# Performance work log

Hardware: AMD Instinct MI355X
Metric: run time of the kernel (lower is better)

Reference implementation:

```python
import jax, jax.numpy as jnp
import numpy as np

B, T = 8, 1024
D = 256          # n_embd
NH = 4           # n_head
MULT = 4         # mlp_internal_dim_multiplier
GRID = 32        # grid_size, T == GRID*GRID
NLAYER = 3
N = D * MULT // NH   # sparse head dim = 256
EPS = 1e-5


def _freqs_2d(h, w, dim, theta=10000.0):
    # matches get_freqs_2d_fixed: returns (h*w, dim//2) complex64
    dim_half = dim // 2
    freqs = 1.0 / theta ** (np.arange(0, dim_half, 2, dtype=np.float32) / dim_half)
    fx = np.outer(np.arange(w, dtype=np.float32), freqs)
    fy = np.outer(np.arange(h, dtype=np.float32), freqs)
    cx = np.exp(1j * fx).astype(np.complex64)          # (w, dim_half/2)
    cy = np.exp(1j * fy).astype(np.complex64)          # (h, dim_half/2)
    gx = np.broadcast_to(cx[None, :, :], (h, w, cx.shape[-1]))
    gy = np.broadcast_to(cy[:, None, :], (h, w, cy.shape[-1]))
    return np.concatenate([gx, gy], axis=-1).reshape(h * w, -1)

FREQS = jnp.asarray(_freqs_2d(GRID, GRID, N))  # (T, N//2) complex64


def _rope(x):
    # x: (B, nh, T, N) real -> complex pairs, rotate, back to real
    xc = x.reshape(*x.shape[:-1], -1, 2)
    xc = jax.lax.complex(xc[..., 0], xc[..., 1])       # (B, nh, T, N/2)
    xr = xc * FREQS[None, None, :, :]
    out = jnp.stack([jnp.real(xr), jnp.imag(xr)], axis=-1)
    return out.reshape(x.shape).astype(x.dtype)


def _ln(x):
    # LayerNorm over last dim, no affine (biased variance, like torch)
    m = jnp.mean(x, axis=-1, keepdims=True)
    v = jnp.var(x, axis=-1, keepdims=True)
    return (x - m) / jnp.sqrt(v + EPS)


def setup_inputs() -> dict:
    key = jax.random.key(0)
    ks = jax.random.split(key, 6)
    std = 0.02
    return {
        "inputs": jax.random.normal(ks[0], (B, T), dtype=jnp.float32),
        "in_w": jax.random.normal(ks[1], (D, 1), dtype=jnp.float32) * std,
        "in_b": jnp.zeros((D,), dtype=jnp.float32),
        "encoder": jax.random.normal(ks[2], (NH, D, N), dtype=jnp.float32) * std,
        "encoder_v": jax.random.normal(ks[3], (NH, D, N), dtype=jnp.float32) * std,
        "decoder": jax.random.normal(ks[4], (NH * N, D), dtype=jnp.float32) * std,
        "out_w": jax.random.normal(ks[5], (1, D), dtype=jnp.float32) * std,
        "out_b": jnp.zeros((1,), dtype=jnp.float32),
    }


def reference(inputs, in_w, in_b, encoder, encoder_v, decoder, out_w, out_b):
    # input projection: (B,T,1) @ (1,D) + b -> (B,T,D)
    x = inputs[..., None] * in_w[None, None, :, 0].swapaxes(-1, -1)  # placeholder
    x = inputs[..., None] @ in_w.T + in_b                            # (B,T,D)
    x = _ln(x)
    scale = 1.0 / jnp.sqrt(jnp.asarray(N, dtype=x.dtype))
    for _ in range(NLAYER):
        # encoder: (B,T,D) x (nh,D,N) -> (B,nh,T,N)
        x_sparse = jax.nn.relu(jnp.einsum('btd,hdn->bhtn', x, encoder))
        QR = _rope(x_sparse)
        KR = _rope(x_sparse)
        scores = jnp.einsum('bhtn,bhsn->bhts', QR, KR) * scale       # (B,nh,T,T)
        attn = jax.nn.softmax(scores, axis=-1)
        yKV = jnp.einsum('bhts,bsd->bhtd', attn, x)                  # V = x, broadcast over heads
        yKV = _ln(yKV)
        y_sparse = jax.nn.relu(jnp.einsum('bhtd,hdn->bhtn', yKV, encoder_v))
        xy_sparse = x_sparse * y_sparse                              # (B,nh,T,N)
        # (B,nh,T,N) -> (B,T,nh*N) @ (nh*N,D) -> (B,T,D)
        yMLP = xy_sparse.transpose(0, 2, 1, 3).reshape(B, T, NH * N) @ decoder
        x = _ln(x + _ln(yMLP))
    logits = x @ out_w.T + out_b                                     # (B,T,1)
    return logits
```

## Files before the change

### kernel.cpp

```cpp
#include <hip/hip_runtime.h>
#include <hip/hip_bf16.h>
#include <math.h>

#define B_ 8
#define T_ 1024
#define D_ 256
#define NH_ 4
#define N_ 256
#define EPS_ 1e-5f

typedef __attribute__((ext_vector_type(8))) short short8_t;
typedef __attribute__((ext_vector_type(4))) float floatx4;

__device__ inline unsigned short f2bf(float f) {
    unsigned u = __builtin_bit_cast(unsigned, f);
    u += 0x7FFFu + ((u >> 16) & 1u);
    return (unsigned short)(u >> 16);
}
__device__ inline float bf2f(unsigned short h) {
    return __builtin_bit_cast(float, (unsigned)h << 16);
}

__device__ inline void gload_lds16(const unsigned short* g, unsigned short* l) {
    __builtin_amdgcn_global_load_lds(
        (const __attribute__((address_space(1))) unsigned int*)g,
        (__attribute__((address_space(3))) unsigned int*)l, 16, 0, 0);
}

__device__ inline float2 block_stats_256(float v, float* red) {
    float s1 = v, s2 = v * v;
    #pragma unroll
    for (int o = 32; o > 0; o >>= 1) { s1 += __shfl_down(s1, o); s2 += __shfl_down(s2, o); }
    int wave = threadIdx.x >> 6, lane = threadIdx.x & 63;
    __syncthreads();
    if (lane == 0) { red[wave] = s1; red[4 + wave] = s2; }
    __syncthreads();
    float S1 = red[0] + red[1] + red[2] + red[3];
    float S2 = red[4] + red[5] + red[6] + red[7];
    float mean = S1 * (1.f / 256.f);
    float var  = S2 * (1.f / 256.f) - mean * mean;
    return make_float2(mean, var);
}

__global__ __launch_bounds__(256) void k_wT(
    const float* __restrict__ in, unsigned short* __restrict__ outh,
    unsigned short* __restrict__ outl, int R, int C)
{
    __shared__ float tile[64][65];
    int c0 = blockIdx.x * 64, r0 = blockIdx.y * 64, h = blockIdx.z;
    in += (size_t)h * R * C;
    for (int i = threadIdx.x; i < 4096; i += 256) {
        int r = i >> 6, c = i & 63;
        tile[r][c] = in[(size_t)(r0 + r) * C + c0 + c];
    }
    __syncthreads();
    for (int i = threadIdx.x; i < 4096; i += 256) {
        int c = i >> 6, r = i & 63;
        float v = tile[r][c];
        unsigned short hb = f2bf(v);
        size_t o = (size_t)(h * C + c0 + c) * R + r0 + r;
        outh[o] = hb;
        outl[o] = f2bf(v - bf2f(hb));
    }
}

__global__ __launch_bounds__(256) void k_input_ln(
    const float* __restrict__ inputs, const float* __restrict__ in_w,
    const float* __restrict__ in_b, float* __restrict__ x,
    unsigned short* __restrict__ xh, unsigned short* __restrict__ xl)
{
    __shared__ float red[8];
    int row = blockIdx.x;
    int d = threadIdx.x;
    float v = inputs[row] * in_w[d] + in_b[d];
    float2 mv = block_stats_256(v, red);
    float o = (v - mv.x) * rsqrtf(mv.y + EPS_);
    size_t idx = (size_t)row * D_ + d;
    x[idx] = o;
    unsigned short hb = f2bf(o);
    xh[idx] = hb;
    xl[idx] = f2bf(o - bf2f(hb));
}

template<int MODE>
__global__ __launch_bounds__(256, 2) void k_gemm_mfma(
    const unsigned short* __restrict__ Ah, const unsigned short* __restrict__ Al,
    const unsigned short* __restrict__ Wh, const unsigned short* __restrict__ Wl,
    const unsigned short* __restrict__ xsh, const unsigned short* __restrict__ xsl,
    unsigned short* __restrict__ outh, unsigned short* __restrict__ outl,
    float* __restrict__ outf,
    unsigned short* __restrict__ qrh, unsigned short* __restrict__ qrl)
{
    constexpr int K = (MODE == 2) ? 1024 : 256;
    __shared__ unsigned short As_h[8 * 512], As_l[8 * 512];
    __shared__ unsigned short Ws_h[8 * 512], Ws_l[8 * 512];
    int tid = threadIdx.x;
    int w = tid >> 6, lane = tid & 63, quad = lane >> 4, l16 = lane & 15;
    int wm = w >> 1, wn = w & 1;
    int m0 = blockIdx.y * 128, n0x = blockIdx.x * 128;
    size_t a_row0, w_row0, out_row0;
    int col0;
    int koff = 0, kend = K;
    if (MODE == 1) {
        int bh = blockIdx.z;
        a_row0 = (size_t)bh * 1024 + m0;
        w_row0 = (size_t)((bh & 3) * 256 + n0x);
        out_row0 = (size_t)(bh >> 2) * 1024 + m0;
        col0 = (bh & 3) * 256 + n0x;
    } else {
        a_row0 = m0; w_row0 = n0x; out_row0 = m0; col0 = n0x;
        if (MODE == 2) { koff = blockIdx.z * 256; kend = koff + 256; }
    }
    floatx4 acc[4][4];
    #pragma unroll
    for (int mt = 0; mt < 4; mt++)
        #pragma unroll
        for (int nt = 0; nt < 4; nt++)
            acc[mt][nt] = (floatx4){0.f, 0.f, 0.f, 0.f};

    const unsigned short* ssrc = (w == 0) ? Ah : (w == 1) ? Al : (w == 2) ? Wh : Wl;
    unsigned short* sdst = (w == 0) ? As_h : (w == 1) ? As_l : (w == 2) ? Ws_h : Ws_l;
    size_t srow0 = (w < 2) ? a_row0 : w_row0;

    for (int k0 = koff; k0 < kend; k0 += 32) {
        #pragma unroll
        for (int rt = 0; rt < 8; rt++) {
            size_t g = (srow0 + rt * 16 + l16) * (size_t)K + k0 + quad * 8;
            gload_lds16(ssrc + g, sdst + rt * 512);
        }
        __syncthreads();
        short8_t afh[4], afl[4], bfh[4], bfl[4];
        #pragma unroll
        for (int mt = 0; mt < 4; mt++) {
            afh[mt] = *(const short8_t*)&As_h[(wm * 4 + mt) * 512 + lane * 8];
            afl[mt] = *(const short8_t*)&As_l[(wm * 4 + mt) * 512 + lane * 8];
        }
        #pragma unroll
        for (int nt = 0; nt < 4; nt++) {
            bfh[nt] = *(const short8_t*)&Ws_h[(wn * 4 + nt) * 512 + lane * 8];
            bfl[nt] = *(const short8_t*)&Ws_l[(wn * 4 + nt) * 512 + lane * 8];
        }
        #pragma unroll
        for (int mt = 0; mt < 4; mt++)
            #pragma unroll
            for (int nt = 0; nt < 4; nt++) {
                acc[mt][nt] = __builtin_amdgcn_mfma_f32_16x16x32_bf16(afh[mt], bfh[nt], acc[mt][nt], 0, 0, 0);
                acc[mt][nt] = __builtin_amdgcn_mfma_f32_16x16x32_bf16(afh[mt], bfl[nt], acc[mt][nt], 0, 0, 0);
                acc[mt][nt] = __builtin_amdgcn_mfma_f32_16x16x32_bf16(afl[mt], bfh[nt], acc[mt][nt], 0, 0, 0);
            }
        __syncthreads();
    }

    #pragma unroll
    for (int mt = 0; mt < 4; mt++) {
        #pragma unroll
        for (int r = 0; r < 4; r++) {
            size_t grow = out_row0 + wm * 64 + mt * 16 + quad * 4 + r;
            #pragma unroll
            for (int nt = 0; nt < 4; nt++) {
                int gcol = col0 + wn * 64 + nt * 16 + l16;
                float v = acc[mt][nt][r];
                if (MODE == 0) {
                    v = fmaxf(v, 0.f);
                    size_t o = grow * 1024 + gcol;
                    unsigned short hb = f2bf(v);
                    outh[o] = hb;
                    outl[o] = f2bf(v - bf2f(hb));
                    float vp = __shfl_xor(v, 1);
                    int n = gcol & 255, h = gcol >> 8;
                    int t = (int)(grow & 1023), b = (int)(grow >> 10);
                    int p = n >> 1, j = p & 63;
                    int pos = (p < 64) ? (t & 31) : (t >> 5);
                    float f = __expf((float)j * -0.14391156f);
                    float ang = (float)pos * f;
                    float sn = __sinf(ang), cs = __cosf(ang);
                    float ro = (n & 1) ? (vp * sn + v * cs) : (v * cs - vp * sn);
                    size_t qo = (((size_t)b * NH_ + h) * T_ + t) * N_ + n;
                    unsigned short qb = f2bf(ro);
                    qrh[qo] = qb;
                    qrl[qo] = f2bf(ro - bf2f(qb));
                } else if (MODE == 1) {
                    float y = fmaxf(v, 0.f);
                    size_t o = grow * 1024 + gcol;
                    float xv = bf2f(xsh[o]) + bf2f(xsl[o]);
                    float p = xv * y;
                    unsigned short hb = f2bf(p);
                    outh[o] = hb;
                    outl[o] = f2bf(p - bf2f(hb));
                } else {
                    outf[(size_t)blockIdx.z * 2097152 + grow * 256 + gcol] = v;
                }
            }
        }
    }
}

__global__ __launch_bounds__(256) void k_xT(const float* __restrict__ x,
                                            unsigned short* __restrict__ Vfh,
                                            unsigned short* __restrict__ Vfl)
{
    __shared__ float tile[64][65];
    int t0 = blockIdx.x * 64, d0 = blockIdx.y * 64, b = blockIdx.z;
    const float* src = x + ((size_t)b * T_ + t0) * D_ + d0;
    for (int i = threadIdx.x; i < 1024; i += 256) {
        int r = i >> 4, c = i & 15;
        float4 v = *(const float4*)(src + (size_t)r * D_ + c * 4);
        tile[r][c * 4 + 0] = v.x;
        tile[r][c * 4 + 1] = v.y;
        tile[r][c * 4 + 2] = v.z;
        tile[r][c * 4 + 3] = v.w;
    }
    __syncthreads();
    for (int i = threadIdx.x; i < 1024; i += 256) {
        int d = i >> 4, c = i & 15;
        int tg = t0 + c * 4;
        int jj = tg >> 5, qd = (tg >> 3) & 3, i8 = tg & 7;
        int dg = d0 + d;
        int tn = dg >> 4, s16 = dg & 15;
        size_t o = (((size_t)b * 32 + jj) * 16 + tn) * 512 + (qd * 16 + s16) * 8 + i8;
        float v0 = tile[c * 4 + 0][d], v1 = tile[c * 4 + 1][d];
        float v2 = tile[c * 4 + 2][d], v3 = tile[c * 4 + 3][d];
        ushort4 oh, ol;
        oh.x = f2bf(v0); ol.x = f2bf(v0 - bf2f(oh.x));
        oh.y = f2bf(v1); ol.y = f2bf(v1 - bf2f(oh.y));
        oh.z = f2bf(v2); ol.z = f2bf(v2 - bf2f(oh.z));
        oh.w = f2bf(v3); ol.w = f2bf(v3 - bf2f(oh.w));
        *(ushort4*)(Vfh + o) = oh;
        *(ushort4*)(Vfl + o) = ol;
    }
}

#define PPW2 36

__global__ __launch_bounds__(512, 1) void k_attn_mfma(
    const unsigned short* __restrict__ qr_h, const unsigned short* __restrict__ qr_l,
    const unsigned short* __restrict__ Vf_h, const unsigned short* __restrict__ Vf_l,
    unsigned short* __restrict__ ykvh, unsigned short* __restrict__ ykvl)
{
    __shared__ unsigned short K_h[2][16 * 512];
    __shared__ unsigned short K_l[2][16 * 512];
    __shared__ unsigned short V_h[2][16 * 512];
    __shared__ unsigned short V_l[2][16 * 512];
    __shared__ unsigned short P_h[4][32 * PPW2];
    __shared__ unsigned short P_l[4][32 * PPW2];
    __shared__ float l_scr[8][32];
    __shared__ float s1_scr[8][32];
    __shared__ float s2_scr[8][32];

    int tid = threadIdx.x;
    int w = tid >> 6, lane = tid & 63, quad = lane >> 4, l16 = lane & 15;
    int rg = w >> 1, half = w & 1;
    int gid = blockIdx.x;
    int bh = gid & 31, tile = gid >> 5, b = bh >> 2;
    int t0q = tile * 128;
    const unsigned short* qhb = qr_h + (size_t)bh * T_ * N_;
    const unsigned short* qlb = qr_l + (size_t)bh * T_ * N_;
    const unsigned short* vhb = Vf_h + (size_t)b * 32 * 16 * 512;
    const unsigned short* vlb = Vf_l + (size_t)b * 32 * 16 * 512;

    short8_t qfh[2][8], qfl[2][8];
    #pragma unroll
    for (int mt = 0; mt < 2; mt++)
        #pragma unroll
        for (int kc = 0; kc < 8; kc++) {
            size_t o = (size_t)(t0q + rg * 32 + mt * 16 + l16) * N_ + kc * 32 + quad * 8;
            qfh[mt][kc] = *(const short8_t*)(qhb + o);
            qfl[mt][kc] = *(const short8_t*)(qlb + o);
        }

    floatx4 O[2][8];
    #pragma unroll
    for (int mt = 0; mt < 2; mt++)
        #pragma unroll
        for (int t = 0; t < 8; t++) O[mt][t] = (floatx4){0.f, 0.f, 0.f, 0.f};
    float lst[2][4] = {{0.f, 0.f, 0.f, 0.f}, {0.f, 0.f, 0.f, 0.f}};
    const float scale = 0.0625f;

    #pragma unroll
    for (int s = 0; s < 2; s++) {
        int slot = w * 2 + s;
        int ct = slot >> 3, kc = slot & 7;
        size_t go = (size_t)(ct * 16 + l16) * N_ + kc * 32 + quad * 8;
        gload_lds16(qhb + go, &K_h[0][slot * 512]);
        gload_lds16(qlb + go, &K_l[0][slot * 512]);
        size_t vo = ((size_t)slot << 9) + lane * 8;
        gload_lds16(vhb + vo, &V_h[0][slot * 512]);
        gload_lds16(vlb + vo, &V_l[0][slot * 512]);
    }

    for (int j = 0; j < 32; j++) {
        int buf = j & 1;
        __syncthreads();
        if (j < 31) {
            #pragma unroll
            for (int s = 0; s < 2; s++) {
                int slot = w * 2 + s;
                size_t vo = ((size_t)((j + 1) * 16 + slot) << 9) + lane * 8;
                gload_lds16(vhb + vo, &V_h[buf ^ 1][slot * 512]);
                gload_lds16(vlb + vo, &V_l[buf ^ 1][slot * 512]);
            }
        }

        floatx4 a_hh0 = (floatx4){0.f, 0.f, 0.f, 0.f};
        floatx4 a_hl0 = (floatx4){0.f, 0.f, 0.f, 0.f};
        floatx4 a_lh0 = (floatx4){0.f, 0.f, 0.f, 0.f};
        floatx4 a_hh1 = (floatx4){0.f, 0.f, 0.f, 0.f};
        floatx4 a_hl1 = (floatx4){0.f, 0.f, 0.f, 0.f};
        floatx4 a_lh1 = (floatx4){0.f, 0.f, 0.f, 0.f};
        __builtin_amdgcn_s_setprio(1);
        #pragma unroll
        for (int kc = 0; kc < 8; kc++) {
            short8_t bkh = *(const short8_t*)&K_h[buf][(half * 8 + kc) * 512 + lane * 8];
            short8_t bkl = *(const short8_t*)&K_l[buf][(half * 8 + kc) * 512 + lane * 8];
            a_hh0 = __builtin_amdgcn_mfma_f32_16x16x32_bf16(qfh[0][kc], bkh, a_hh0, 0, 0, 0);
            a_hh1 = __builtin_amdgcn_mfma_f32_16x16x32_bf16(qfh[1][kc], bkh, a_hh1, 0, 0, 0);
            a_hl0 = __builtin_amdgcn_mfma_f32_16x16x32_bf16(qfh[0][kc], bkl, a_hl0, 0, 0, 0);
            a_hl1 = __builtin_amdgcn_mfma_f32_16x16x32_bf16(qfh[1][kc], bkl, a_hl1, 0, 0, 0);
            a_lh0 = __builtin_amdgcn_mfma_f32_16x16x32_bf16(qfl[0][kc], bkh, a_lh0, 0, 0, 0);
            a_lh1 = __builtin_amdgcn_mfma_f32_16x16x32_bf16(qfl[1][kc], bkh, a_lh1, 0, 0, 0);
        }
        __builtin_amdgcn_s_setprio(0);
        floatx4 sc0 = (a_hh0 + a_hl0) + a_lh0;
        floatx4 sc1 = (a_hh1 + a_hl1) + a_lh1;

        #pragma unroll
        for (int r = 0; r < 4; r++) {
            float p0 = __expf(sc0[r] * scale - 8.f);
            float p1 = __expf(sc1[r] * scale - 8.f);
            lst[0][r] += p0;
            lst[1][r] += p1;
            int row0 = quad * 4 + r, row1 = 16 + quad * 4 + r;
            unsigned short p0h = f2bf(p0), p1h = f2bf(p1);
            P_h[rg][row0 * PPW2 + half * 16 + l16] = p0h;
            P_h[rg][row1 * PPW2 + half * 16 + l16] = p1h;
            P_l[rg][row0 * PPW2 + half * 16 + l16] = f2bf(p0 - bf2f(p0h));
            P_l[rg][row1 * PPW2 + half * 16 + l16] = f2bf(p1 - bf2f(p1h));
        }

        __syncthreads();
        if (j < 31) {
            #pragma unroll
            for (int s = 0; s < 2; s++) {
                int slot = w * 2 + s;
                int ct = slot >> 3, kc = slot & 7;
                size_t go = (size_t)((j + 1) * 32 + ct * 16 + l16) * N_ + kc * 32 + quad * 8;
                gload_lds16(qhb + go, &K_h[buf ^ 1][slot * 512]);
                gload_lds16(qlb + go, &K_l[buf ^ 1][slot * 512]);
            }
        }

        short8_t pah0 = *(const short8_t*)&P_h[rg][(l16) * PPW2 + quad * 8];
        short8_t pal0 = *(const short8_t*)&P_l[rg][(l16) * PPW2 + quad * 8];
        short8_t pah1 = *(const short8_t*)&P_h[rg][(16 + l16) * PPW2 + quad * 8];
        short8_t pal1 = *(const short8_t*)&P_l[rg][(16 + l16) * PPW2 + quad * 8];

        __builtin_amdgcn_s_setprio(1);
        #pragma unroll
        for (int t = 0; t < 8; t++) {
            int tn = half * 8 + t;
            short8_t vbh = *(const short8_t*)&V_h[buf][tn * 512 + lane * 8];
            short8_t vbl = *(const short8_t*)&V_l[buf][tn * 512 + lane * 8];
            O[0][t] = __builtin_amdgcn_mfma_f32_16x16x32_bf16(pah0, vbh, O[0][t], 0, 0, 0);
            O[1][t] = __builtin_amdgcn_mfma_f32_16x16x32_bf16(pah1, vbh, O[1][t], 0, 0, 0);
            O[0][t] = __builtin_amdgcn_mfma_f32_16x16x32_bf16(pah0, vbl, O[0][t], 0, 0, 0);
            O[1][t] = __builtin_amdgcn_mfma_f32_16x16x32_bf16(pah1, vbl, O[1][t], 0, 0, 0);
            O[0][t] = __builtin_amdgcn_mfma_f32_16x16x32_bf16(pal0, vbh, O[0][t], 0, 0, 0);
            O[1][t] = __builtin_amdgcn_mfma_f32_16x16x32_bf16(pal1, vbh, O[1][t], 0, 0, 0);
        }
        __builtin_amdgcn_s_setprio(0);
    }

    #pragma unroll
    for (int mt = 0; mt < 2; mt++)
        #pragma unroll
        for (int r = 0; r < 4; r++) {
            float ls = lst[mt][r];
            #pragma unroll
            for (int o = 1; o < 16; o <<= 1) ls += __shfl_xor(ls, o);
            float s1 = 0.f, s2 = 0.f;
            #pragma unroll
            for (int t = 0; t < 8; t++) { float v = O[mt][t][r]; s1 += v; s2 += v * v; }
            #pragma unroll
            for (int o = 1; o < 16; o <<= 1) { s1 += __shfl_xor(s1, o); s2 += __shfl_xor(s2, o); }
            int row = mt * 16 + quad * 4 + r;
            if (l16 == 0) { l_scr[w][row] = ls; s1_scr[w][row] = s1; s2_scr[w][row] = s2; }
        }
    __syncthreads();
    #pragma unroll
    for (int mt = 0; mt < 2; mt++)
        #pragma unroll
        for (int r = 0; r < 4; r++) {
            int row = mt * 16 + quad * 4 + r;
            float ls = l_scr[w][row] + l_scr[w ^ 1][row];
            float s1 = s1_scr[w][row] + s1_scr[w ^ 1][row];
            float s2 = s2_scr[w][row] + s2_scr[w ^ 1][row];
            float li = 1.f / ls;
            float mean = s1 * li * (1.f / 256.f);
            float e2   = s2 * li * li * (1.f / 256.f);
            float var  = e2 - mean * mean;
            float rs = rsqrtf(var + EPS_);
            float a = li * rs, bb = mean * rs;
            size_t obase = ((size_t)bh * T_ + t0q + rg * 32 + row) * D_;
            #pragma unroll
            for (int t = 0; t < 8; t++) {
                float v = O[mt][t][r] * a - bb;
                size_t o = obase + half * 128 + t * 16 + l16;
                unsigned short hb = f2bf(v);
                ykvh[o] = hb;
                ykvl[o] = f2bf(v - bf2f(hb));
            }
        }
}

__global__ __launch_bounds__(256) void k_resid_ln(float* __restrict__ x,
                                                  const float* __restrict__ ymlp,
                                                  unsigned short* __restrict__ xh,
                                                  unsigned short* __restrict__ xl)
{
    __shared__ float red[8];
    int row = blockIdx.x, d = threadIdx.x;
    size_t o = (size_t)row * D_ + d;
    float y = ymlp[o] + ymlp[o + 2097152] + ymlp[o + 2 * 2097152] + ymlp[o + 3 * 2097152];
    float2 mv1 = block_stats_256(y, red);
    float v = x[o] + (y - mv1.x) * rsqrtf(mv1.y + EPS_);
    float2 mv2 = block_stats_256(v, red);
    float out = (v - mv2.x) * rsqrtf(mv2.y + EPS_);
    x[o] = out;
    unsigned short hb = f2bf(out);
    xh[o] = hb;
    xl[o] = f2bf(out - bf2f(hb));
}

__global__ __launch_bounds__(256) void k_logits(
    const float* __restrict__ x, const float* __restrict__ out_w,
    const float* __restrict__ out_b, float* __restrict__ out)
{
    __shared__ float red[4];
    int row = blockIdx.x, d = threadIdx.x;
    float v = x[(size_t)row * D_ + d] * out_w[d];
    #pragma unroll
    for (int o = 32; o > 0; o >>= 1) v += __shfl_down(v, o);
    int wave = d >> 6, lane = d & 63;
    if (lane == 0) red[wave] = v;
    __syncthreads();
    if (d == 0) out[row] = red[0] + red[1] + red[2] + red[3] + out_b[0];
}

extern "C" void kernel_launch(void* const* d_in, const int* in_sizes, int n_in,
                              void* d_out, int out_size, void* d_ws, size_t ws_size,
                              hipStream_t stream)
{
    (void)in_sizes; (void)n_in; (void)out_size;
    if (ws_size < ((size_t)115 << 20)) return;

    const float* inputs    = (const float*)d_in[0];
    const float* in_w      = (const float*)d_in[1];
    const float* in_b      = (const float*)d_in[2];
    const float* encoder   = (const float*)d_in[3];
    const float* encoder_v = (const float*)d_in[4];
    const float* decoder   = (const float*)d_in[5];
    const float* out_w     = (const float*)d_in[6];
    const float* out_b     = (const float*)d_in[7];

    char* wsb = (char*)d_ws;
    float* x             = (float*)(wsb);
    unsigned short* x_h  = (unsigned short*)(wsb + ((size_t)8  << 20));
    unsigned short* x_l  = (unsigned short*)(wsb + ((size_t)12 << 20));
    unsigned short* Vf_h = x_h;
    unsigned short* Vf_l = x_l;
    unsigned short* xs_h = (unsigned short*)(wsb + ((size_t)16 << 20));
    unsigned short* xs_l = (unsigned short*)(wsb + ((size_t)32 << 20));
    float* ymlp          = (float*)(wsb + ((size_t)16 << 20));
    unsigned short* qr_h = (unsigned short*)(wsb + ((size_t)48 << 20));
    unsigned short* qr_l = (unsigned short*)(wsb + ((size_t)64 << 20));
    unsigned short* xy_h = qr_h;
    unsigned short* xy_l = qr_l;
    unsigned short* ykv_h = (unsigned short*)(wsb + ((size_t)80 << 20));
    unsigned short* ykv_l = (unsigned short*)(wsb + ((size_t)96 << 20));
    char* wbase = wsb + ((size_t)112 << 20);
    unsigned short* encT_h = (unsigned short*)(wbase);
    unsigned short* encT_l = (unsigned short*)(wbase + 0x80000);
    unsigned short* evT_h  = (unsigned short*)(wbase + 2 * 0x80000);
    unsigned short* evT_l  = (unsigned short*)(wbase + 3 * 0x80000);
    unsigned short* decT_h = (unsigned short*)(wbase + 4 * 0x80000);
    unsigned short* decT_l = (unsigned short*)(wbase + 5 * 0x80000);

    k_wT<<<dim3(4, 4, 4), 256, 0, stream>>>(encoder,   encT_h, encT_l, 256, 256);
    k_wT<<<dim3(4, 4, 4), 256, 0, stream>>>(encoder_v, evT_h,  evT_l,  256, 256);
    k_wT<<<dim3(4, 16, 1), 256, 0, stream>>>(decoder,  decT_h, decT_l, 1024, 256);

    k_input_ln<<<B_ * T_, 256, 0, stream>>>(inputs, in_w, in_b, x, x_h, x_l);
    for (int l = 0; l < 3; l++) {
        k_gemm_mfma<0><<<dim3(8, 64, 1), 256, 0, stream>>>(
            x_h, x_l, encT_h, encT_l, nullptr, nullptr, xs_h, xs_l, nullptr, qr_h, qr_l);
        k_xT<<<dim3(16, 4, 8), 256, 0, stream>>>(x, Vf_h, Vf_l);
        k_attn_mfma<<<256, 512, 0, stream>>>(qr_h, qr_l, Vf_h, Vf_l, ykv_h, ykv_l);
        k_gemm_mfma<1><<<dim3(2, 8, 32), 256, 0, stream>>>(
            ykv_h, ykv_l, evT_h, evT_l, xs_h, xs_l, xy_h, xy_l, nullptr, nullptr, nullptr);
        k_gemm_mfma<2><<<dim3(2, 64, 4), 256, 0, stream>>>(
            xy_h, xy_l, decT_h, decT_l, nullptr, nullptr, nullptr, nullptr, ymlp, nullptr, nullptr);
        k_resid_ln<<<B_ * T_, 256, 0, stream>>>(x, ymlp, x_h, x_l);
    }
    k_logits<<<B_ * T_, 256, 0, stream>>>(x, out_w, out_b, (float*)d_out);
}
```

Before: 732.4 us.

## Fuse encoder_v GEMM, gating product, and decoder GEMM into one kernel

Replaces the separate encoder_v GEMM (MODE 1) and decoder GEMM (MODE 2) with one fused kernel. Each 512-thread block computes a full 128x256 y_sparse tile, multiplies it by x_sparse, and writes the bf16 hi/lo product straight into LDS as the A operand of the decoder GEMM, so the xy_sparse tensor never round-trips through global memory. Both GEMM phases use double-buffered LDS staging so global loads overlap MFMA. The cost is a grid of only 256 blocks at one block per CU, larger LDS use, and per-head partial outputs that resid_ln still has to sum.

```diff
diff --git a/kernel.cpp b/kernel.cpp
--- a/kernel.cpp
+++ b/kernel.cpp
@@ -86,31 +86,18 @@
 __global__ __launch_bounds__(256, 2) void k_gemm_mfma(
     const unsigned short* __restrict__ Ah, const unsigned short* __restrict__ Al,
     const unsigned short* __restrict__ Wh, const unsigned short* __restrict__ Wl,
-    const unsigned short* __restrict__ xsh, const unsigned short* __restrict__ xsl,
     unsigned short* __restrict__ outh, unsigned short* __restrict__ outl,
-    float* __restrict__ outf,
     unsigned short* __restrict__ qrh, unsigned short* __restrict__ qrl)
 {
-    constexpr int K = (MODE == 2) ? 1024 : 256;
+    constexpr int K = 256;
     __shared__ unsigned short As_h[8 * 512], As_l[8 * 512];
     __shared__ unsigned short Ws_h[8 * 512], Ws_l[8 * 512];
     int tid = threadIdx.x;
     int w = tid >> 6, lane = tid & 63, quad = lane >> 4, l16 = lane & 15;
     int wm = w >> 1, wn = w & 1;
     int m0 = blockIdx.y * 128, n0x = blockIdx.x * 128;
-    size_t a_row0, w_row0, out_row0;
-    int col0;
-    int koff = 0, kend = K;
-    if (MODE == 1) {
-        int bh = blockIdx.z;
-        a_row0 = (size_t)bh * 1024 + m0;
-        w_row0 = (size_t)((bh & 3) * 256 + n0x);
-        out_row0 = (size_t)(bh >> 2) * 1024 + m0;
-        col0 = (bh & 3) * 256 + n0x;
-    } else {
-        a_row0 = m0; w_row0 = n0x; out_row0 = m0; col0 = n0x;
-        if (MODE == 2) { koff = blockIdx.z * 256; kend = koff + 256; }
-    }
+    size_t a_row0 = m0, w_row0 = n0x, out_row0 = m0;
+    int col0 = n0x;
     floatx4 acc[4][4];
     #pragma unroll
     for (int mt = 0; mt < 4; mt++)
@@ -122,7 +109,7 @@
     unsigned short* sdst = (w == 0) ? As_h : (w == 1) ? As_l : (w == 2) ? Ws_h : Ws_l;
     size_t srow0 = (w < 2) ? a_row0 : w_row0;
 
-    for (int k0 = koff; k0 < kend; k0 += 32) {
+    for (int k0 = 0; k0 < K; k0 += 32) {
         #pragma unroll
         for (int rt = 0; rt < 8; rt++) {
             size_t g = (srow0 + rt * 16 + l16) * (size_t)K + k0 + quad * 8;
@@ -160,39 +147,170 @@
             for (int nt = 0; nt < 4; nt++) {
                 int gcol = col0 + wn * 64 + nt * 16 + l16;
                 float v = acc[mt][nt][r];
-                if (MODE == 0) {
-                    v = fmaxf(v, 0.f);
-                    size_t o = grow * 1024 + gcol;
-                    unsigned short hb = f2bf(v);
-                    outh[o] = hb;
-                    outl[o] = f2bf(v - bf2f(hb));
-                    float vp = __shfl_xor(v, 1);
-                    int n = gcol & 255, h = gcol >> 8;
-                    int t = (int)(grow & 1023), b = (int)(grow >> 10);
-                    int p = n >> 1, j = p & 63;
-                    int pos = (p < 64) ? (t & 31) : (t >> 5);
-                    float f = __expf((float)j * -0.14391156f);
-                    float ang = (float)pos * f;
-                    float sn = __sinf(ang), cs = __cosf(ang);
-                    float ro = (n & 1) ? (vp * sn + v * cs) : (v * cs - vp * sn);
-                    size_t qo = (((size_t)b * NH_ + h) * T_ + t) * N_ + n;
-                    unsigned short qb = f2bf(ro);
-                    qrh[qo] = qb;
-                    qrl[qo] = f2bf(ro - bf2f(qb));
-                } else if (MODE == 1) {
-                    float y = fmaxf(v, 0.f);
+                v = fmaxf(v, 0.f);
+                size_t o = grow * 1024 + gcol;
+                unsigned short hb = f2bf(v);
+                outh[o] = hb;
+                outl[o] = f2bf(v - bf2f(hb));
+                float vp = __shfl_xor(v, 1);
+                int n = gcol & 255, h = gcol >> 8;
+                int t = (int)(grow & 1023), b = (int)(grow >> 10);
+                int p = n >> 1, j = p & 63;
+                int pos = (p < 64) ? (t & 31) : (t >> 5);
+                float f = __expf((float)j * -0.14391156f);
+                float ang = (float)pos * f;
+                float sn = __sinf(ang), cs = __cosf(ang);
+                float ro = (n & 1) ? (vp * sn + v * cs) : (v * cs - vp * sn);
+                size_t qo = (((size_t)b * NH_ + h) * T_ + t) * N_ + n;
+                unsigned short qb = f2bf(ro);
+                qrh[qo] = qb;
+                qrl[qo] = f2bf(ro - bf2f(qb));
+            }
+        }
+    }
+}
+
+__global__ __launch_bounds__(512, 1) void k_gemm_fused(
+    const unsigned short* __restrict__ Ah, const unsigned short* __restrict__ Al,
+    const unsigned short* __restrict__ Wh, const unsigned short* __restrict__ Wl,
+    const unsigned short* __restrict__ D2h, const unsigned short* __restrict__ D2l,
+    const unsigned short* __restrict__ xsh, const unsigned short* __restrict__ xsl,
+    float* __restrict__ outf)
+{
+    __shared__ unsigned short SM[2][24576];
+    int tid = threadIdx.x;
+    int w = tid >> 6, lane = tid & 63, quad = lane >> 4, l16 = lane & 15;
+    int wm = w >> 2, wn = w & 3;
+    int m0 = blockIdx.x * 128;
+    int bh = blockIdx.y, b = bh >> 2, h = bh & 3;
+    size_t a_row0 = (size_t)bh * 1024 + m0;
+    size_t w_row0 = (size_t)h * 256;
+    size_t xrow0  = (size_t)b * 1024 + m0;
+
+    floatx4 acc[4][4];
+    #pragma unroll
+    for (int mt = 0; mt < 4; mt++)
+        #pragma unroll
+        for (int nt = 0; nt < 4; nt++)
+            acc[mt][nt] = (floatx4){0.f, 0.f, 0.f, 0.f};
+
+    auto stage_main = [&](int k0, int bw) {
+        #pragma unroll
+        for (int t = 0; t < 6; t++) {
+            int idx = w * 6 + t;
+            const unsigned short* src; unsigned short* dst; size_t rowb; int rt;
+            if (idx < 8)       { rt = idx;      src = Ah; dst = &SM[bw][0];     rowb = a_row0; }
+            else if (idx < 16) { rt = idx - 8;  src = Al; dst = &SM[bw][4096];  rowb = a_row0; }
+            else if (idx < 32) { rt = idx - 16; src = Wh; dst = &SM[bw][8192];  rowb = w_row0; }
+            else               { rt = idx - 32; src = Wl; dst = &SM[bw][16384]; rowb = w_row0; }
+            gload_lds16(src + (rowb + rt * 16 + l16) * 256 + k0 + quad * 8, dst + rt * 512);
+        }
+    };
+
+    stage_main(0, 0);
+    for (int s = 0; s < 8; s++) {
+        int buf = s & 1;
+        __syncthreads();
+        if (s < 7) stage_main((s + 1) * 32, buf ^ 1);
+        short8_t afh[4], afl[4], bfh[4], bfl[4];
+        #pragma unroll
+        for (int mt = 0; mt < 4; mt++) {
+            afh[mt] = *(const short8_t*)&SM[buf][(wm * 4 + mt) * 512 + lane * 8];
+            afl[mt] = *(const short8_t*)&SM[buf][4096 + (wm * 4 + mt) * 512 + lane * 8];
+        }
+        #pragma unroll
+        for (int nt = 0; nt < 4; nt++) {
+            bfh[nt] = *(const short8_t*)&SM[buf][8192  + (wn * 4 + nt) * 512 + lane * 8];
+            bfl[nt] = *(const short8_t*)&SM[buf][16384 + (wn * 4 + nt) * 512 + lane * 8];
+        }
+        #pragma unroll
+        for (int mt = 0; mt < 4; mt++)
+            #pragma unroll
+            for (int nt = 0; nt < 4; nt++) {
+                acc[mt][nt] = __builtin_amdgcn_mfma_f32_16x16x32_bf16(afh[mt], bfh[nt], acc[mt][nt], 0, 0, 0);
+                acc[mt][nt] = __builtin_amdgcn_mfma_f32_16x16x32_bf16(afh[mt], bfl[nt], acc[mt][nt], 0, 0, 0);
+                acc[mt][nt] = __builtin_amdgcn_mfma_f32_16x16x32_bf16(afl[mt], bfh[nt], acc[mt][nt], 0, 0, 0);
+            }
+    }
+
+    auto write_xy = [&](int c, int bw) {
+        if (wn != (c >> 1)) return;
+        int cb = c & 1;
+        #pragma unroll
+        for (int mt = 0; mt < 4; mt++)
+            #pragma unroll
+            for (int nt = 0; nt < 4; nt++) {
+                if ((nt >> 1) != cb) continue;
+                #pragma unroll
+                for (int r = 0; r < 4; r++) {
+                    float v = fmaxf(acc[mt][nt][r], 0.f);
+                    size_t grow = xrow0 + wm * 64 + mt * 16 + quad * 4 + r;
+                    int gcol = h * 256 + wn * 64 + nt * 16 + l16;
                     size_t o = grow * 1024 + gcol;
                     float xv = bf2f(xsh[o]) + bf2f(xsl[o]);
-                    float p = xv * y;
-                    unsigned short hb = f2bf(p);
-                    outh[o] = hb;
-                    outl[o] = f2bf(p - bf2f(hb));
-                } else {
-                    outf[(size_t)blockIdx.z * 2097152 + grow * 256 + gcol] = v;
+                    float p = xv * v;
+                    unsigned short ph = f2bf(p);
+                    int kin = (nt & 1) * 16 + l16;
+                    int ad = (wm * 4 + mt) * 512 + (kin >> 3) * 128 + (quad * 4 + r) * 8 + (kin & 7);
+                    SM[bw][ad] = ph;
+                    SM[bw][4096 + ad] = f2bf(p - bf2f(ph));
                 }
             }
-        }
-    }
+    };
+    auto stage_w2 = [&](int c, int bw) {
+        #pragma unroll
+        for (int t = 0; t < 4; t++) {
+            int idx = w * 4 + t;
+            const unsigned short* src = (idx < 16) ? D2h : D2l;
+            unsigned short* dst = (idx < 16) ? &SM[bw][8192] : &SM[bw][16384];
+            int rt = idx & 15;
+            gload_lds16(src + (size_t)(rt * 16 + l16) * 1024 + h * 256 + c * 32 + quad * 8,
+                        dst + rt * 512);
+        }
+    };
+
+    floatx4 acc2[4][4];
+    #pragma unroll
+    for (int mt = 0; mt < 4; mt++)
+        #pragma unroll
+        for (int nt = 0; nt < 4; nt++)
+            acc2[mt][nt] = (floatx4){0.f, 0.f, 0.f, 0.f};
+
+    write_xy(0, 0);
+    stage_w2(0, 0);
+    #pragma unroll
+    for (int c = 0; c < 8; c++) {
+        int buf = c & 1;
+        __syncthreads();
+        if (c < 7) { write_xy(c + 1, buf ^ 1); stage_w2(c + 1, buf ^ 1); }
+        short8_t b2h[4], b2l[4];
+        #pragma unroll
+        for (int nt = 0; nt < 4; nt++) {
+            b2h[nt] = *(const short8_t*)&SM[buf][8192  + (wn * 4 + nt) * 512 + lane * 8];
+            b2l[nt] = *(const short8_t*)&SM[buf][16384 + (wn * 4 + nt) * 512 + lane * 8];
+        }
+        #pragma unroll
+        for (int mt = 0; mt < 4; mt++) {
+            short8_t a2h = *(const short8_t*)&SM[buf][(wm * 4 + mt) * 512 + lane * 8];
+            short8_t a2l = *(const short8_t*)&SM[buf][4096 + (wm * 4 + mt) * 512 + lane * 8];
+            #pragma unroll
+            for (int nt = 0; nt < 4; nt++) {
+                acc2[mt][nt] = __builtin_amdgcn_mfma_f32_16x16x32_bf16(a2h, b2h[nt], acc2[mt][nt], 0, 0, 0);
+                acc2[mt][nt] = __builtin_amdgcn_mfma_f32_16x16x32_bf16(a2h, b2l[nt], acc2[mt][nt], 0, 0, 0);
+                acc2[mt][nt] = __builtin_amdgcn_mfma_f32_16x16x32_bf16(a2l, b2h[nt], acc2[mt][nt], 0, 0, 0);
+            }
+        }
+    }
+
+    #pragma unroll
+    for (int mt = 0; mt < 4; mt++)
+        #pragma unroll
+        for (int r = 0; r < 4; r++) {
+            size_t grow = xrow0 + wm * 64 + mt * 16 + quad * 4 + r;
+            #pragma unroll
+            for (int nt = 0; nt < 4; nt++)
+                outf[(size_t)h * 2097152 + grow * 256 + wn * 64 + nt * 16 + l16] = acc2[mt][nt][r];
+        }
 }
 
 __global__ __launch_bounds__(256) void k_xT(const float* __restrict__ x,
@@ -470,11 +588,9 @@
     unsigned short* Vf_l = x_l;
     unsigned short* xs_h = (unsigned short*)(wsb + ((size_t)16 << 20));
     unsigned short* xs_l = (unsigned short*)(wsb + ((size_t)32 << 20));
-    float* ymlp          = (float*)(wsb + ((size_t)16 << 20));
     unsigned short* qr_h = (unsigned short*)(wsb + ((size_t)48 << 20));
     unsigned short* qr_l = (unsigned short*)(wsb + ((size_t)64 << 20));
-    unsigned short* xy_h = qr_h;
-    unsigned short* xy_l = qr_l;
+    float* ymlp          = (float*)(wsb + ((size_t)48 << 20));
     unsigned short* ykv_h = (unsigned short*)(wsb + ((size_t)80 << 20));
     unsigned short* ykv_l = (unsigned short*)(wsb + ((size_t)96 << 20));
     char* wbase = wsb + ((size_t)112 << 20);
@@ -492,13 +608,11 @@
     k_input_ln<<<B_ * T_, 256, 0, stream>>>(inputs, in_w, in_b, x, x_h, x_l);
     for (int l = 0; l < 3; l++) {
         k_gemm_mfma<0><<<dim3(8, 64, 1), 256, 0, stream>>>(
-            x_h, x_l, encT_h, encT_l, nullptr, nullptr, xs_h, xs_l, nullptr, qr_h, qr_l);
+            x_h, x_l, encT_h, encT_l, xs_h, xs_l, qr_h, qr_l);
         k_xT<<<dim3(16, 4, 8), 256, 0, stream>>>(x, Vf_h, Vf_l);
         k_attn_mfma<<<256, 512, 0, stream>>>(qr_h, qr_l, Vf_h, Vf_l, ykv_h, ykv_l);
-        k_gemm_mfma<1><<<dim3(2, 8, 32), 256, 0, stream>>>(
-            ykv_h, ykv_l, evT_h, evT_l, xs_h, xs_l, xy_h, xy_l, nullptr, nullptr, nullptr);
-        k_gemm_mfma<2><<<dim3(2, 64, 4), 256, 0, stream>>>(
-            xy_h, xy_l, decT_h, decT_l, nullptr, nullptr, nullptr, nullptr, ymlp, nullptr, nullptr);
+        k_gemm_fused<<<dim3(8, 32), 512, 0, stream>>>(
+            ykv_h, ykv_l, evT_h, evT_l, decT_h, decT_l, xs_h, xs_l, ymlp);
         k_resid_ln<<<B_ * T_, 256, 0, stream>>>(x, ymlp, x_h, x_l);
     }
     k_logits<<<B_ * T_, 256, 0, stream>>>(x, out_w, out_b, (float*)d_out);
```

Measured after the change: 937.2 us. 1.28x slower.
